# Kernel tuning notes

Hardware: AMD Instinct MI355X
Metric: run time of the kernel (lower is better)

Reference implementation:

```python
import jax, jax.numpy as jnp
import numpy as np

B, N, C, D, H, L, F = 64, 256, 16, 512, 8, 8, 2048
HD = D // H
PI = np.pi


def _ln(x, w, b, eps=1e-5):
    mu = jnp.mean(x, -1, keepdims=True)
    var = jnp.mean(jnp.square(x - mu), -1, keepdims=True)
    return (x - mu) * jax.lax.rsqrt(var + eps) * w + b


def _forward(x_node, x_full, Wp, bp, cls, e_w1, e_b1, e_w2, e_b2, edge_scale,
             qkv_w, qkv_b, out_w, out_b, ln1_w, ln1_b, ln2_w, ln2_b,
             ff1_w, ff1_b, ff2_w, ff2_b, cl_ln_w, cl_ln_b, cl_w1, cl_b1, cl_w2, cl_b2):
    Bq, Nq, _ = x_node.shape
    # pairwise kaon geometry from absolute y/phi
    y = x_full[:, :, 14]
    phi = x_full[:, :, 15]
    dy = jnp.abs(y[:, :, None] - y[:, None, :])                                  # [B,N,N]
    dphi = jnp.abs(jnp.mod(phi[:, :, None] - phi[:, None, :] + PI, 2 * PI) - PI)
    dr = jnp.sqrt(dy * dy + dphi * dphi + 1e-8)
    ef = jnp.stack([dy, dphi, dr], -1)                                           # [B,N,N,3]
    hmid = jax.nn.gelu(ef @ e_w1.T + e_b1, approximate=False)                    # [B,N,N,16]
    raw = hmid @ e_w2.T + e_b2                                                   # [B,N,N,H]
    central = jnp.mean(raw, axis=2).transpose(0, 2, 1)                           # [B,H,N]
    edge_bias = raw.transpose(0, 3, 1, 2)                                        # [B,H,N,N]
    bias = jnp.zeros((Bq, H, Nq + 1, Nq + 1), x_node.dtype)
    bias = bias.at[:, :, 1:, 1:].set(edge_bias)
    bias = bias.at[:, :, 0, 1:].set(central * edge_scale)
    bias = bias.at[:, :, 1:, 0].set(central * edge_scale)

    h = x_node @ Wp.T + bp
    h = jnp.concatenate([jnp.broadcast_to(cls, (Bq, 1, D)), h], axis=1)          # [B,S,D]
    S = Nq + 1
    scale = 1.0 / np.sqrt(HD)
    for l in range(L):  # pre-norm TransformerEncoderLayer (activation=relu, no final norm)
        x = _ln(h, ln1_w[l], ln1_b[l])
        qkv = x @ qkv_w[l].T + qkv_b[l]
        q, k, v = jnp.split(qkv, 3, axis=-1)
        q = q.reshape(Bq, S, H, HD).transpose(0, 2, 1, 3)
        k = k.reshape(Bq, S, H, HD).transpose(0, 2, 1, 3)
        v = v.reshape(Bq, S, H, HD).transpose(0, 2, 1, 3)
        scores = jnp.einsum('bhqd,bhkd->bhqk', q, k) * scale + bias
        attn = jax.nn.softmax(scores, axis=-1)
        o = jnp.einsum('bhqk,bhkd->bhqd', attn, v).transpose(0, 2, 1, 3).reshape(Bq, S, D)
        h = h + o @ out_w[l].T + out_b[l]
        x = _ln(h, ln2_w[l], ln2_b[l])
        h = h + jax.nn.relu(x @ ff1_w[l].T + ff1_b[l]) @ ff2_w[l].T + ff2_b[l]
    x = _ln(h[:, 0], cl_ln_w, cl_ln_b)
    return jax.nn.gelu(x @ cl_w1.T + cl_b1, approximate=False) @ cl_w2.T + cl_b2  # [B,2]


def setup_inputs() -> dict:
    key = jax.random.key(0)
    ks = iter(jax.random.split(key, 40))
    f32 = jnp.float32

    def nrm(shape, s=0.02):
        return (s * jax.random.normal(next(ks), shape)).astype(f32)

    return {
        'x_node': jax.random.normal(next(ks), (B, N, C), f32),
        'x_full': jax.random.normal(next(ks), (B, N, 16), f32),
        'Wp': nrm((D, C)), 'bp': jnp.zeros((D,), f32),
        'cls': nrm((1, 1, D)),
        'e_w1': nrm((16, 3), 0.3), 'e_b1': jnp.zeros((16,), f32),
        'e_w2': nrm((H, 16), 0.01), 'e_b2': jnp.zeros((H,), f32),
        'edge_scale': jnp.full((1,), 0.1, f32),
        'qkv_w': nrm((L, 3 * D, D)), 'qkv_b': jnp.zeros((L, 3 * D), f32),
        'out_w': nrm((L, D, D)), 'out_b': jnp.zeros((L, D), f32),
        'ln1_w': jnp.ones((L, D), f32), 'ln1_b': jnp.zeros((L, D), f32),
        'ln2_w': jnp.ones((L, D), f32), 'ln2_b': jnp.zeros((L, D), f32),
        'ff1_w': nrm((L, F, D)), 'ff1_b': jnp.zeros((L, F), f32),
        'ff2_w': nrm((L, D, F)), 'ff2_b': jnp.zeros((L, D), f32),
        'cl_ln_w': jnp.ones((D,), f32), 'cl_ln_b': jnp.zeros((D,), f32),
        'cl_w1': nrm((D // 2, D)), 'cl_b1': jnp.zeros((D // 2,), f32),
        'cl_w2': nrm((2, D // 2)), 'cl_b2': jnp.zeros((2,), f32),
    }


def reference(x_node, x_full, Wp, bp, cls, e_w1, e_b1, e_w2, e_b2, edge_scale,
              qkv_w, qkv_b, out_w, out_b, ln1_w, ln1_b, ln2_w, ln2_b,
              ff1_w, ff1_b, ff2_w, ff2_b, cl_ln_w, cl_ln_b, cl_w1, cl_b1, cl_w2, cl_b2):
    return _forward(x_node, x_full, Wp, bp, cls, e_w1, e_b1, e_w2, e_b2, edge_scale,
                    qkv_w, qkv_b, out_w, out_b, ln1_w, ln1_b, ln2_w, ln2_b,
                    ff1_w, ff1_b, ff2_w, ff2_b, cl_ln_w, cl_ln_b, cl_w1, cl_b1, cl_w2, cl_b2)
```

## Files before the change

kernel.cpp:

```cpp
#include <hip/hip_runtime.h>
#include <hip/hip_bf16.h>
#include <stdint.h>

#define PI_F     3.14159265358979323846f
#define TWO_PI_F 6.28318530717958647692f
#define INV2PI_F 0.15915494309189535f

typedef __attribute__((ext_vector_type(8))) short bf16x8;
typedef __attribute__((ext_vector_type(4))) float f32x4;

#define BB 64
#define NN 256
#define SS 257
#define DD 512
#define HH 8
#define HDD 64
#define LL 8
#define MTOK 16448
#define MPAD 16512
#define BSTR 264
#define VSTR 320

__device__ __forceinline__ float b2f(unsigned short u){
  union { float f; uint32_t i; } c; c.i = ((uint32_t)u) << 16; return c.f;
}
__device__ __forceinline__ unsigned short f2b(float f){
  union { float f; uint32_t i; } c; c.f = f;
  uint32_t r = c.i + 0x7FFFu + ((c.i >> 16) & 1u);
  return (unsigned short)(r >> 16);
}
__device__ __forceinline__ float gelu_fast(float z){
  const float z2 = z*z;
  const float u2 = z * (1.5957691216f + 0.071354816f*z2);
  const float e = __expf(u2);
  const float r = __builtin_amdgcn_rcpf(1.f + e);
  const float th = 1.f - 2.f*r;
  return 0.5f*z*(1.f + th);
}

typedef __attribute__((address_space(1))) unsigned char ga_t;
typedef __attribute__((address_space(3))) unsigned char ls_t;
__device__ __forceinline__ void gl_lds16(const void* g, void* l){
  __builtin_amdgcn_global_load_lds((ga_t*)g, (ls_t*)l, 16, 0, 0);
}

__global__ __launch_bounds__(256) void cvt_kernel(const float* __restrict__ src,
                                                  unsigned short* __restrict__ dst, int n2){
  int i = blockIdx.x*256 + threadIdx.x;
  int stride = gridDim.x*256;
  for (; i < n2; i += stride){
    float2 v = ((const float2*)src)[i];
    ((uint32_t*)dst)[i] = (uint32_t)f2b(v.x) | ((uint32_t)f2b(v.y) << 16);
  }
}

__global__ __launch_bounds__(256) void edge_kernel(
    const float* __restrict__ x_full, const float* __restrict__ e_w1, const float* __restrict__ e_b1,
    const float* __restrict__ e_w2, const float* __restrict__ e_b2,
    unsigned short* __restrict__ bias, float* __restrict__ central)
{
  const int bi = blockIdx.x;
  const int b = bi >> 8, i = bi & 255;
  const int j = threadIdx.x;
  const float yi = x_full[((long)b*NN + i)*16 + 14];
  const float fi = x_full[((long)b*NN + i)*16 + 15];
  const float yj = x_full[((long)b*NN + j)*16 + 14];
  const float fj = x_full[((long)b*NN + j)*16 + 15];
  const float dy = fabsf(yi - yj);
  const float xw = fi - fj + PI_F;
  const float tw = xw * INV2PI_F;
  const float md = (tw - floorf(tw)) * TWO_PI_F;
  const float dphi = fabsf(md - PI_F);
  const float dr = sqrtf(dy*dy + dphi*dphi + 1e-8f);
  float raw[8];
  #pragma unroll
  for (int hh = 0; hh < 8; ++hh) raw[hh] = e_b2[hh];
  #pragma unroll
  for (int k = 0; k < 16; ++k){
    float z = e_w1[k*3]*dy + e_w1[k*3+1]*dphi + e_w1[k*3+2]*dr + e_b1[k];
    float g = gelu_fast(z);
    #pragma unroll
    for (int hh = 0; hh < 8; ++hh) raw[hh] += g * e_w2[hh*16 + k];
  }
  #pragma unroll
  for (int hh = 0; hh < 8; ++hh)
    bias[(((long)b*HH + hh)*SS + 1 + i)*BSTR + 1 + j] = f2b(raw[hh]);
  #pragma unroll
  for (int m = 1; m < 64; m <<= 1)
    #pragma unroll
    for (int hh = 0; hh < 8; ++hh) raw[hh] += __shfl_xor(raw[hh], m);
  __shared__ float cw[4][8];
  const int wv = j >> 6;
  if ((j & 63) == 0)
    for (int hh = 0; hh < 8; ++hh) cw[wv][hh] = raw[hh];
  __syncthreads();
  if (j < 8){
    float t = cw[0][j] + cw[1][j] + cw[2][j] + cw[3][j];
    central[((long)b*NN + i)*HH + j] = t * (1.f/NN);
  }
}

__global__ __launch_bounds__(256) void edge_border_kernel(
    const float* __restrict__ central, const float* __restrict__ edge_scale,
    unsigned short* __restrict__ bias)
{
  const int bh = blockIdx.x;
  const int b = bh >> 3, h = bh & 7;
  const int j = threadIdx.x;
  const float es = edge_scale[0];
  const float cv = central[((long)b*NN + j)*HH + h] * es;
  const long base = (long)bh*SS*BSTR;
  const unsigned short u = f2b(cv);
  bias[base + 1 + j] = u;
  bias[base + (long)(1+j)*BSTR] = u;
  if (j == 0) bias[base] = 0;
}

__global__ __launch_bounds__(256) void proj_kernel(
    const float* __restrict__ x_node, const float* __restrict__ Wp,
    const float* __restrict__ bp, const float* __restrict__ cls, float* __restrict__ hb)
{
  const int t = blockIdx.x;
  const int tid = threadIdx.x;
  const int b = t / SS, s2 = t - b*SS;
  float2 o;
  if (s2 == 0){
    o = *(const float2*)(cls + tid*2);
  } else {
    const float* xr = x_node + ((long)b*NN + (s2-1))*16;
    float xv[16];
    #pragma unroll
    for (int c2 = 0; c2 < 16; ++c2) xv[c2] = xr[c2];
    float oo[2];
    #pragma unroll
    for (int e = 0; e < 2; ++e){
      int d = tid*2 + e;
      float a = bp[d];
      const float* wr2 = Wp + (long)d*16;
      #pragma unroll
      for (int c2 = 0; c2 < 16; ++c2) a += xv[c2]*wr2[c2];
      oo[e] = a;
    }
    o.x = oo[0]; o.y = oo[1];
  }
  *(float2*)(hb + (long)t*DD + tid*2) = o;
}

__global__ __launch_bounds__(256) void ln_kernel(
    const float* __restrict__ hb, const float* __restrict__ w,
    const float* __restrict__ bbv, unsigned short* __restrict__ xb)
{
  const int tok = blockIdx.x*4 + (threadIdx.x >> 6);
  const int lane = threadIdx.x & 63;
  const float4* p = (const float4*)(hb + (long)tok*DD + lane*8);
  const float4 a = p[0], bq = p[1];
  float s  = a.x + a.y + a.z + a.w + bq.x + bq.y + bq.z + bq.w;
  float ss = a.x*a.x + a.y*a.y + a.z*a.z + a.w*a.w
           + bq.x*bq.x + bq.y*bq.y + bq.z*bq.z + bq.w*bq.w;
  #pragma unroll
  for (int m = 1; m < 64; m <<= 1){ s += __shfl_xor(s, m); ss += __shfl_xor(ss, m); }
  const float mu = s * (1.f/DD);
  const float var = ss * (1.f/DD) - mu*mu;
  const float rs = rsqrtf(var + 1e-5f);
  const float4* wp = (const float4*)(w + lane*8);
  const float4* bp2 = (const float4*)(bbv + lane*8);
  const float4 w0 = wp[0], w1 = wp[1];
  const float4 b0 = bp2[0], b1 = bp2[1];
  bf16x8 o;
  o[0] = (short)f2b((a.x - mu)*rs*w0.x + b0.x);
  o[1] = (short)f2b((a.y - mu)*rs*w0.y + b0.y);
  o[2] = (short)f2b((a.z - mu)*rs*w0.z + b0.z);
  o[3] = (short)f2b((a.w - mu)*rs*w0.w + b0.w);
  o[4] = (short)f2b((bq.x - mu)*rs*w1.x + b1.x);
  o[5] = (short)f2b((bq.y - mu)*rs*w1.y + b1.y);
  o[6] = (short)f2b((bq.z - mu)*rs*w1.z + b1.z);
  o[7] = (short)f2b((bq.w - mu)*rs*w1.w + b1.w);
  *(bf16x8*)(xb + (long)tok*DD + lane*8) = o;
}

template<int EPI, int MI, int NI, int WPE>
__global__ __launch_bounds__(256, WPE) void gemm_kernel(
    const unsigned short* __restrict__ A, const unsigned short* __restrict__ Bw,
    const float* __restrict__ bias, void* __restrict__ Cout,
    int M, int N, int K, int ldc, int nblocks)
{
  __shared__ __align__(16) char smem[MI*4096 + NI*4096];
  unsigned short* As = (unsigned short*)smem;
  unsigned short* Bs = (unsigned short*)(smem + MI*4096);
  const int tid = threadIdx.x;
  const int lane = tid & 63;
  const int wave = tid >> 6;
  const int wr = wave >> 1, wc = wave & 1;
  const int l16 = lane & 15, lhi = lane >> 4;

  const int nwg = gridDim.x;
  const int q8 = nwg >> 3, r8 = nwg & 7;
  const int xcd = blockIdx.x & 7, idx = blockIdx.x >> 3;
  const int lin = (xcd < r8 ? xcd*(q8+1) : r8*(q8+1) + (xcd-r8)*q8) + idx;
  const int mb = lin / nblocks;
  const int nb = lin - mb*nblocks;
  const long m0 = (long)mb * (MI*32);
  const long n0 = (long)nb * (NI*32);

  f32x4 acc[MI][NI];
  const f32x4 z4 = {0.f, 0.f, 0.f, 0.f};
  #pragma unroll
  for (int mi = 0; mi < MI; ++mi)
    #pragma unroll
    for (int ni = 0; ni < NI; ++ni) acc[mi][ni] = z4;

  const char* Ab = (const char*)A;
  const char* Bb = (const char*)Bw;
  const int nkt = K >> 6;
  for (int kt = 0; kt < nkt; ++kt){
    #pragma unroll
    for (int c = 0; c < MI; ++c){
      const int bo = c*4096 + tid*16;
      const int row = bo >> 7;
      const int kb = bo & 127;
      gl_lds16(Ab + ((m0+row)*(long)K)*2 + (long)kt*128 + kb, (char*)As + bo);
    }
    #pragma unroll
    for (int c = 0; c < NI; ++c){
      const int bo = c*4096 + tid*16;
      const int row = bo >> 7;
      const int kb = bo & 127;
      gl_lds16(Bb + ((n0+row)*(long)K)*2 + (long)kt*128 + kb, (char*)Bs + bo);
    }
    __syncthreads();
    #pragma unroll
    for (int kd = 0; kd < 2; ++kd){
      bf16x8 af[MI], bfr[NI];
      #pragma unroll
      for (int mi = 0; mi < MI; ++mi)
        af[mi] = *(const bf16x8*)((const char*)As + (wr*(MI*16) + mi*16 + l16)*128 + kd*64 + lhi*16);
      #pragma unroll
      for (int ni = 0; ni < NI; ++ni)
        bfr[ni] = *(const bf16x8*)((const char*)Bs + (wc*(NI*16) + ni*16 + l16)*128 + kd*64 + lhi*16);
      #pragma unroll
      for (int mi = 0; mi < MI; ++mi)
        #pragma unroll
        for (int ni = 0; ni < NI; ++ni)
          acc[mi][ni] = __builtin_amdgcn_mfma_f32_16x16x32_bf16(af[mi], bfr[ni], acc[mi][ni], 0, 0, 0);
    }
    __syncthreads();
  }

  if (EPI == 2){
    float* Cs = (float*)smem;
    const int NC = NI*32;
    const int LDSC = NC + 4;
    float* Cg = (float*)Cout;
    #pragma unroll
    for (int half = 0; half < 2; ++half){
      if (wr == half){
        #pragma unroll
        for (int mi = 0; mi < MI; ++mi)
          #pragma unroll
          for (int ni = 0; ni < NI; ++ni){
            const int col = wc*(NI*16) + ni*16 + l16;
            #pragma unroll
            for (int r = 0; r < 4; ++r)
              Cs[(mi*16 + lhi*4 + r)*LDSC + col] = acc[mi][ni][r];
          }
      }
      __syncthreads();
      #pragma unroll
      for (int it = 0; it < MI; ++it){
        const int idx = tid + it*256;
        const int c4 = idx & 15;
        const int row = idx >> 4;
        const int gm = (int)m0 + half*(MI*16) + row;
        if (gm < M){
          const long go = (long)gm*ldc + n0 + c4*4;
          float4 cv = *(float4*)&Cg[go];
          const float* ls = &Cs[row*LDSC + c4*4];
          const float4 bv = *(const float4*)&bias[n0 + c4*4];
          cv.x += ls[0] + bv.x; cv.y += ls[1] + bv.y;
          cv.z += ls[2] + bv.z; cv.w += ls[3] + bv.w;
          *(float4*)&Cg[go] = cv;
        }
      }
      __syncthreads();
    }
  } else {
    #pragma unroll
    for (int mi = 0; mi < MI; ++mi){
      #pragma unroll
      for (int ni = 0; ni < NI; ++ni){
        const int col = (int)n0 + wc*(NI*16) + ni*16 + l16;
        const float bn = bias[col];
        const int rowb = (int)m0 + wr*(MI*16) + mi*16 + lhi*4;
        #pragma unroll
        for (int r = 0; r < 4; ++r){
          const int m = rowb + r;
          if (m < M){
            float v = acc[mi][ni][r] + bn;
            if (EPI == 1) v = fmaxf(v, 0.f);
            ((unsigned short*)Cout)[(long)m*ldc + col] = f2b(v);
          }
        }
      }
    }
  }
}

__global__ __launch_bounds__(256) void vtrans_kernel(
    const unsigned short* __restrict__ qkv, unsigned short* __restrict__ vt)
{
  const int bh = blockIdx.x;
  const int c = blockIdx.y;
  const int b = bh >> 3, h = bh & 7;
  __shared__ unsigned short tile[64][72];
  const int tid = threadIdx.x;
  const int rr = tid >> 3, ch = tid & 7;
  #pragma unroll
  for (int it = 0; it < 2; ++it){
    const int sl = it*32 + rr;
    const long tok = (long)b*SS + c*64 + sl;
    bf16x8 v = *(const bf16x8*)(qkv + tok*1536 + 1024 + h*64 + ch*8);
    *(bf16x8*)(&tile[sl][ch*8]) = v;
  }
  __syncthreads();
  #pragma unroll
  for (int it = 0; it < 2; ++it){
    const int d = it*32 + rr;
    const int s0 = c*64 + ch*8;
    bf16x8 o;
    #pragma unroll
    for (int e = 0; e < 8; ++e){
      const int sgl = s0 + e;
      o[e] = (sgl < SS) ? (short)tile[ch*8 + e][d] : (short)0;
    }
    *(bf16x8*)(vt + ((long)bh*HDD + d)*VSTR + s0) = o;
  }
}

__global__ __launch_bounds__(576) void flash_kernel(
    const unsigned short* __restrict__ qkv, const unsigned short* __restrict__ vt,
    const unsigned short* __restrict__ bias, unsigned short* __restrict__ ob)
{
  const int bh = blockIdx.x;
  const int b = bh >> 3, h = bh & 7;
  const int qt = threadIdx.x >> 6;
  const int lane = threadIdx.x & 63;
  const int l16 = lane & 15, lhi = lane >> 4;

  __shared__ unsigned short Ks[2][2048];
  __shared__ unsigned short Vs[2][2048];
  __shared__ unsigned short Bsh[9][2][1024];
  __shared__ unsigned short pt[9][1024];
  unsigned short* ptw = pt[qt];

  bf16x8 qf[2][2];
  #pragma unroll
  for (int mi = 0; mi < 2; ++mi)
    #pragma unroll
    for (int kd = 0; kd < 2; ++kd){
      const long tok = (long)b*SS + qt*32 + mi*16 + l16;
      qf[mi][kd] = *(const bf16x8*)(qkv + tok*1536 + h*64 + kd*32 + lhi*8);
    }

  auto stage = [&](int jtn, int bb){
    const int rB = lane >> 2, cB = lane & 3;
    const char* gb = (const char*)bias + (((long)bh*SS + qt*32)*BSTR + (long)jtn*32)*2;
    char* lb = (char*)&Bsh[qt][bb][0];
    gl_lds16(gb + (long)rB*BSTR*2        + cB*16, lb + lane*16);
    gl_lds16(gb + (long)(16+rB)*BSTR*2   + cB*16, lb + 1024 + lane*16);
    if (qt < 4){
      const int rK = lane >> 3, cK = lane & 7;
      gl_lds16((const char*)qkv + (((long)b*SS + jtn*32 + qt*8 + rK)*1536 + 512 + h*64)*2 + ((cK ^ rK)*16),
               (char*)&Ks[bb][0] + qt*1024 + lane*16);
    } else if (qt < 8){
      const int rV = lane >> 2, cV = lane & 3;
      const int d = (qt-4)*16 + rV;
      gl_lds16((const char*)vt + (((long)bh*64 + d)*VSTR + (long)jtn*32)*2 + ((cV ^ (rV & 3))*16),
               (char*)&Vs[bb][0] + (qt-4)*1024 + lane*16);
    }
  };

  f32x4 oacc[2][4];
  const f32x4 z4 = {0.f, 0.f, 0.f, 0.f};
  #pragma unroll
  for (int mi = 0; mi < 2; ++mi)
    #pragma unroll
    for (int ni = 0; ni < 4; ++ni) oacc[mi][ni] = z4;
  float mrow[2][4], lrow[2][4];
  #pragma unroll
  for (int mi = 0; mi < 2; ++mi)
    #pragma unroll
    for (int r = 0; r < 4; ++r){ mrow[mi][r] = -1e30f; lrow[mi][r] = 0.f; }

  stage(0, 0);
  __builtin_amdgcn_sched_barrier(0);

  for (int jt = 0; jt < 9; ++jt){
    const int cur = jt & 1;
    if (jt < 8){
      stage(jt+1, cur ^ 1);
      __builtin_amdgcn_sched_barrier(0);
      if (qt < 8) asm volatile("s_waitcnt vmcnt(3)" ::: "memory");
      else        asm volatile("s_waitcnt vmcnt(2)" ::: "memory");
    } else {
      asm volatile("s_waitcnt vmcnt(0)" ::: "memory");
    }
    __builtin_amdgcn_sched_barrier(0);
    __builtin_amdgcn_s_barrier();
    __builtin_amdgcn_sched_barrier(0);

    bf16x8 kf[2][2];
    #pragma unroll
    for (int ni = 0; ni < 2; ++ni)
      #pragma unroll
      for (int kd = 0; kd < 2; ++kd){
        const int row = ni*16 + l16;
        const int sw = (kd*4 + lhi) ^ (row & 7);
        kf[ni][kd] = *(const bf16x8*)((const char*)&Ks[cur][0] + row*128 + sw*16);
      }
    f32x4 sacc[2][2];
    #pragma unroll
    for (int mi = 0; mi < 2; ++mi)
      #pragma unroll
      for (int ni = 0; ni < 2; ++ni) sacc[mi][ni] = z4;
    __builtin_amdgcn_s_setprio(1);
    #pragma unroll
    for (int kd = 0; kd < 2; ++kd)
      #pragma unroll
      for (int mi = 0; mi < 2; ++mi)
        #pragma unroll
        for (int ni = 0; ni < 2; ++ni)
          sacc[mi][ni] = __builtin_amdgcn_mfma_f32_16x16x32_bf16(qf[mi][kd], kf[ni][kd], sacc[mi][ni], 0, 0, 0);
    __builtin_amdgcn_s_setprio(0);

    float sv[2][2][4];
    #pragma unroll
    for (int mi = 0; mi < 2; ++mi)
      #pragma unroll
      for (int ni = 0; ni < 2; ++ni)
        #pragma unroll
        for (int r = 0; r < 4; ++r){
          const int col = jt*32 + ni*16 + l16;
          float x = sacc[mi][ni][r] * 0.125f;
          x += b2f(Bsh[qt][cur][(mi*16 + lhi*4 + r)*32 + ni*16 + l16]);
          if (col >= SS) x = -1e30f;
          sv[mi][ni][r] = x;
        }
    #pragma unroll
    for (int mi = 0; mi < 2; ++mi)
      #pragma unroll
      for (int r = 0; r < 4; ++r){
        float pm = fmaxf(sv[mi][0][r], sv[mi][1][r]);
        #pragma unroll
        for (int sh = 1; sh < 16; sh <<= 1) pm = fmaxf(pm, __shfl_xor(pm, sh));
        const float mold = mrow[mi][r];
        const float mnew = fmaxf(mold, pm);
        const float corr = __expf(mold - mnew);
        mrow[mi][r] = mnew;
        float psum = 0.f;
        #pragma unroll
        for (int ni = 0; ni < 2; ++ni){
          const float p = __expf(sv[mi][ni][r] - mnew);
          sv[mi][ni][r] = p;
          psum += p;
        }
        #pragma unroll
        for (int sh = 1; sh < 16; sh <<= 1) psum += __shfl_xor(psum, sh);
        lrow[mi][r] = lrow[mi][r]*corr + psum;
        #pragma unroll
        for (int ni = 0; ni < 4; ++ni) oacc[mi][ni][r] = oacc[mi][ni][r]*corr;
      }
    #pragma unroll
    for (int mi = 0; mi < 2; ++mi)
      #pragma unroll
      for (int ni = 0; ni < 2; ++ni)
        #pragma unroll
        for (int r = 0; r < 4; ++r)
          ptw[(mi*16 + lhi*4 + r)*32 + ni*16 + l16] = f2b(sv[mi][ni][r]);
    bf16x8 pf[2];
    #pragma unroll
    for (int mi = 0; mi < 2; ++mi)
      pf[mi] = *(const bf16x8*)(ptw + (mi*16 + l16)*32 + lhi*8);
    bf16x8 vf[4];
    #pragma unroll
    for (int ni = 0; ni < 4; ++ni){
      const int d = ni*16 + l16;
      const int sw = lhi ^ (d & 3);
      vf[ni] = *(const bf16x8*)((const char*)&Vs[cur][0] + d*64 + sw*16);
    }
    __builtin_amdgcn_s_setprio(1);
    #pragma unroll
    for (int mi = 0; mi < 2; ++mi)
      #pragma unroll
      for (int ni = 0; ni < 4; ++ni)
        oacc[mi][ni] = __builtin_amdgcn_mfma_f32_16x16x32_bf16(pf[mi], vf[ni], oacc[mi][ni], 0, 0, 0);
    __builtin_amdgcn_s_setprio(0);

    __builtin_amdgcn_sched_barrier(0);
    __builtin_amdgcn_s_barrier();
    __builtin_amdgcn_sched_barrier(0);
  }

  #pragma unroll
  for (int mi = 0; mi < 2; ++mi)
    #pragma unroll
    for (int r = 0; r < 4; ++r){
      const int row = qt*32 + mi*16 + lhi*4 + r;
      if (row < SS){
        const float inv = 1.0f / lrow[mi][r];
        const long tok = (long)b*SS + row;
        #pragma unroll
        for (int ni = 0; ni < 4; ++ni)
          ob[tok*DD + h*HDD + ni*16 + l16] = f2b(oacc[mi][ni][r] * inv);
      }
    }
}

__global__ __launch_bounds__(256) void cls_kernel(
    const float* __restrict__ hb, const float* __restrict__ lw, const float* __restrict__ lb,
    const float* __restrict__ w1, const float* __restrict__ b1,
    const float* __restrict__ w2, const float* __restrict__ b2, float* __restrict__ out)
{
  const int b = blockIdx.x;
  const int tid = threadIdx.x;
  const float* row = hb + (long)b*SS*DD;
  const float2 v = *(const float2*)(row + tid*2);
  float s = v.x + v.y, ss = v.x*v.x + v.y*v.y;
  #pragma unroll
  for (int m = 1; m < 64; m <<= 1){ s += __shfl_xor(s, m); ss += __shfl_xor(ss, m); }
  __shared__ float red[8];
  const int wv = tid >> 6;
  if ((tid & 63) == 0){ red[wv] = s; red[4+wv] = ss; }
  __syncthreads();
  s  = red[0]+red[1]+red[2]+red[3];
  ss = red[4]+red[5]+red[6]+red[7];
  const float mu = s * (1.f/DD);
  const float var = ss * (1.f/DD) - mu*mu;
  const float rs = rsqrtf(var + 1e-5f);
  __shared__ __align__(16) float xs[DD];
  xs[tid*2]   = (v.x - mu)*rs*lw[tid*2]   + lb[tid*2];
  xs[tid*2+1] = (v.y - mu)*rs*lw[tid*2+1] + lb[tid*2+1];
  __syncthreads();
  float a = b1[tid];
  const float4* w1v = (const float4*)(w1 + (long)tid*DD);
  const float4* xsv = (const float4*)xs;
  for (int d4 = 0; d4 < DD/4; ++d4){
    const float4 wv4 = w1v[d4], xv4 = xsv[d4];
    a += wv4.x*xv4.x + wv4.y*xv4.y + wv4.z*xv4.z + wv4.w*xv4.w;
  }
  const float g = 0.5f*a*(1.f + erff(a*0.70710678118f));
  float p0 = g * w2[tid];
  float p1 = g * w2[256 + tid];
  #pragma unroll
  for (int m = 1; m < 64; m <<= 1){ p0 += __shfl_xor(p0, m); p1 += __shfl_xor(p1, m); }
  __shared__ float r2[8];
  if ((tid & 63) == 0){ r2[wv] = p0; r2[4+wv] = p1; }
  __syncthreads();
  if (tid == 0) out[b*2]   = r2[0]+r2[1]+r2[2]+r2[3] + b2[0];
  if (tid == 1) out[b*2+1] = r2[4]+r2[5]+r2[6]+r2[7] + b2[1];
}

extern "C" void kernel_launch(void* const* d_in, const int* in_sizes, int n_in,
                              void* d_out, int out_size, void* d_ws, size_t ws_size,
                              hipStream_t stream) {
  const float* x_node    = (const float*)d_in[0];
  const float* x_full    = (const float*)d_in[1];
  const float* Wp        = (const float*)d_in[2];
  const float* bp        = (const float*)d_in[3];
  const float* cls       = (const float*)d_in[4];
  const float* e_w1      = (const float*)d_in[5];
  const float* e_b1      = (const float*)d_in[6];
  const float* e_w2      = (const float*)d_in[7];
  const float* e_b2      = (const float*)d_in[8];
  const float* edge_scale= (const float*)d_in[9];
  const float* qkv_w     = (const float*)d_in[10];
  const float* qkv_b     = (const float*)d_in[11];
  const float* out_w     = (const float*)d_in[12];
  const float* out_b     = (const float*)d_in[13];
  const float* ln1_w     = (const float*)d_in[14];
  const float* ln1_b     = (const float*)d_in[15];
  const float* ln2_w     = (const float*)d_in[16];
  const float* ln2_b     = (const float*)d_in[17];
  const float* ff1_w     = (const float*)d_in[18];
  const float* ff1_b     = (const float*)d_in[19];
  const float* ff2_w     = (const float*)d_in[20];
  const float* ff2_b     = (const float*)d_in[21];
  const float* cl_ln_w   = (const float*)d_in[22];
  const float* cl_ln_b   = (const float*)d_in[23];
  const float* cl_w1     = (const float*)d_in[24];
  const float* cl_b1     = (const float*)d_in[25];
  const float* cl_w2     = (const float*)d_in[26];
  const float* cl_b2     = (const float*)d_in[27];
  float* out = (float*)d_out;

  char* w = (char*)d_ws;
  size_t off = 0;
  auto take = [&](size_t bytes)->char*{
    char* p = w + off;
    off += (bytes + 255) & ~(size_t)255;
    return p;
  };
  unsigned short* wq8   = (unsigned short*)take((size_t)LL*1536*512*2);
  unsigned short* wo8   = (unsigned short*)take((size_t)LL*512*512*2);
  unsigned short* wf1   = (unsigned short*)take((size_t)LL*2048*512*2);
  unsigned short* wf2   = (unsigned short*)take((size_t)LL*512*2048*2);
  unsigned short* bias16= (unsigned short*)take((size_t)BB*HH*SS*BSTR*2 + 65536);
  float*          cent  = (float*)take((size_t)BB*NN*HH*4);
  float*          hbuf  = (float*)take((size_t)MPAD*DD*4);
  unsigned short* xb    = (unsigned short*)take((size_t)MPAD*DD*2);
  unsigned short* obuf  = (unsigned short*)take((size_t)MPAD*DD*2);
  unsigned short* qkvb  = (unsigned short*)take((size_t)MPAD*1536*2);
  unsigned short* vtb   = (unsigned short*)take((size_t)BB*HH*HDD*VSTR*2);
  unsigned short* ffb   = qkvb;

  cvt_kernel<<<4096, 256, 0, stream>>>(qkv_w, wq8, LL*1536*512/2);
  cvt_kernel<<<4096, 256, 0, stream>>>(out_w, wo8, LL*512*512/2);
  cvt_kernel<<<4096, 256, 0, stream>>>(ff1_w, wf1, LL*2048*512/2);
  cvt_kernel<<<4096, 256, 0, stream>>>(ff2_w, wf2, LL*512*2048/2);

  edge_kernel<<<dim3(BB*NN), 256, 0, stream>>>(x_full, e_w1, e_b1, e_w2, e_b2, bias16, cent);
  edge_border_kernel<<<dim3(BB*HH), 256, 0, stream>>>(cent, edge_scale, bias16);
  proj_kernel<<<dim3(MTOK), 256, 0, stream>>>(x_node, Wp, bp, cls, hbuf);

  for (int l = 0; l < LL; ++l){
    ln_kernel<<<dim3(MTOK/4), 256, 0, stream>>>(hbuf, ln1_w + l*DD, ln1_b + l*DD, xb);
    gemm_kernel<0,4,4,4><<<dim3(129*12), 256, 0, stream>>>(xb, wq8 + (size_t)l*1536*512,
        qkv_b + (size_t)l*1536, qkvb, MTOK, 1536, 512, 1536, 12);
    vtrans_kernel<<<dim3(512, 5), 256, 0, stream>>>(qkvb, vtb);
    flash_kernel<<<dim3(512), 576, 0, stream>>>(qkvb, vtb, bias16, obuf);
    gemm_kernel<2,4,2,6><<<dim3(129*8), 256, 0, stream>>>(obuf, wo8 + (size_t)l*512*512,
        out_b + (size_t)l*DD, hbuf, MTOK, 512, 512, 512, 8);
    ln_kernel<<<dim3(MTOK/4), 256, 0, stream>>>(hbuf, ln2_w + l*DD, ln2_b + l*DD, xb);
    gemm_kernel<1,4,4,4><<<dim3(129*16), 256, 0, stream>>>(xb, wf1 + (size_t)l*2048*512,
        ff1_b + (size_t)l*2048, ffb, MTOK, 2048, 512, 2048, 16);
    gemm_kernel<2,4,2,6><<<dim3(129*8), 256, 0, stream>>>(ffb, wf2 + (size_t)l*512*2048,
        ff2_b + (size_t)l*DD, hbuf, MTOK, 512, 2048, 512, 8);
  }
  cls_kernel<<<dim3(BB), 256, 0, stream>>>(hbuf, cl_ln_w, cl_ln_b, cl_w1, cl_b1, cl_w2, cl_b2, out);
}
```

Measured before the change: 2.530 ms.

## Prepack attention bias into MFMA fragment layout and load it into registers

A new one-time kernel repacks the padded bf16 attention bias into per-tile, per-lane MFMA accumulator order. The flash kernel then reads each lane's bias values with two coalesced 16-byte register loads, prefetched one KV tile ahead, instead of staging bias through shared memory and reading it back element by element. This removes the large bias LDS buffer, so more of the CU's shared memory is free and the LDS traffic per tile drops. In exchange there are more live registers, a larger bias workspace, and the original bias and output buffers now alias the qkv and LN-output workspaces.

```diff
diff --git a/kernel.cpp b/kernel.cpp
--- a/kernel.cpp
+++ b/kernel.cpp
@@ -114,6 +114,28 @@
   bias[base + 1 + j] = u;
   bias[base + (long)(1+j)*BSTR] = u;
   if (j == 0) bias[base] = 0;
+}
+
+__global__ __launch_bounds__(256) void brepack_kernel(
+    const unsigned short* __restrict__ biasO, unsigned short* __restrict__ biasT)
+{
+  const int bh = blockIdx.x;
+  const int qt = blockIdx.y;
+  const int t = threadIdx.x;
+  const int ln = t & 63, wv = t >> 6;
+  const int l16 = ln & 15, lhi = ln >> 4;
+  for (int c = wv; c < 18; c += 4){
+    const int jt = c >> 1, mi = c & 1;
+    bf16x8 v;
+    #pragma unroll
+    for (int idx8 = 0; idx8 < 8; ++idx8){
+      const int ni = idx8 >> 2, r = idx8 & 3;
+      int row = qt*32 + mi*16 + lhi*4 + r; if (row > 256) row = 256;
+      int col = jt*32 + ni*16 + l16;       if (col > 263) col = 263;
+      v[idx8] = (short)biasO[((long)bh*SS + row)*BSTR + col];
+    }
+    *(bf16x8*)(biasT + ((((long)bh*9 + qt)*9 + jt)*2 + mi)*512 + ln*8) = v;
+  }
 }
 
 __global__ __launch_bounds__(256) void proj_kernel(
@@ -338,7 +360,7 @@
 
 __global__ __launch_bounds__(576) void flash_kernel(
     const unsigned short* __restrict__ qkv, const unsigned short* __restrict__ vt,
-    const unsigned short* __restrict__ bias, unsigned short* __restrict__ ob)
+    const unsigned short* __restrict__ biasT, unsigned short* __restrict__ ob)
 {
   const int bh = blockIdx.x;
   const int b = bh >> 3, h = bh & 7;
@@ -348,7 +370,6 @@
 
   __shared__ unsigned short Ks[2][2048];
   __shared__ unsigned short Vs[2][2048];
-  __shared__ unsigned short Bsh[9][2][1024];
   __shared__ unsigned short pt[9][1024];
   unsigned short* ptw = pt[qt];
 
@@ -362,11 +383,6 @@
     }
 
   auto stage = [&](int jtn, int bb){
-    const int rB = lane >> 2, cB = lane & 3;
-    const char* gb = (const char*)bias + (((long)bh*SS + qt*32)*BSTR + (long)jtn*32)*2;
-    char* lb = (char*)&Bsh[qt][bb][0];
-    gl_lds16(gb + (long)rB*BSTR*2        + cB*16, lb + lane*16);
-    gl_lds16(gb + (long)(16+rB)*BSTR*2   + cB*16, lb + 1024 + lane*16);
     if (qt < 4){
       const int rK = lane >> 3, cK = lane & 7;
       gl_lds16((const char*)qkv + (((long)b*SS + jtn*32 + qt*8 + rK)*1536 + 512 + h*64)*2 + ((cK ^ rK)*16),
@@ -379,6 +395,12 @@
     }
   };
 
+  const long tqb = ((long)bh*9 + qt)*9;
+  bf16x8 btA0, btA1, btB0, btB1;
+  btA0 = *(const bf16x8*)(biasT + (tqb + 0)*1024 + lane*8);
+  btA1 = *(const bf16x8*)(biasT + (tqb + 0)*1024 + 512 + lane*8);
+  btB0 = btA0; btB1 = btA1;
+
   f32x4 oacc[2][4];
   const f32x4 z4 = {0.f, 0.f, 0.f, 0.f};
   #pragma unroll
@@ -398,6 +420,14 @@
     const int cur = jt & 1;
     if (jt < 8){
       stage(jt+1, cur ^ 1);
+      const long tbn = (tqb + (jt+1))*1024;
+      if (cur){
+        btA0 = *(const bf16x8*)(biasT + tbn + lane*8);
+        btA1 = *(const bf16x8*)(biasT + tbn + 512 + lane*8);
+      } else {
+        btB0 = *(const bf16x8*)(biasT + tbn + lane*8);
+        btB1 = *(const bf16x8*)(biasT + tbn + 512 + lane*8);
+      }
       __builtin_amdgcn_sched_barrier(0);
       if (qt < 8) asm volatile("s_waitcnt vmcnt(3)" ::: "memory");
       else        asm volatile("s_waitcnt vmcnt(2)" ::: "memory");
@@ -407,6 +437,9 @@
     __builtin_amdgcn_sched_barrier(0);
     __builtin_amdgcn_s_barrier();
     __builtin_amdgcn_sched_barrier(0);
+
+    const bf16x8 bt0 = cur ? btB0 : btA0;
+    const bf16x8 bt1 = cur ? btB1 : btA1;
 
     bf16x8 kf[2][2];
     #pragma unroll
@@ -441,7 +474,7 @@
         for (int r = 0; r < 4; ++r){
           const int col = jt*32 + ni*16 + l16;
           float x = sacc[mi][ni][r] * 0.125f;
-          x += b2f(Bsh[qt][cur][(mi*16 + lhi*4 + r)*32 + ni*16 + l16]);
+          x += b2f((unsigned short)((mi ? bt1 : bt0)[ni*4 + r]));
           if (col >= SS) x = -1e30f;
           sv[mi][ni][r] = x;
         }
@@ -603,14 +636,15 @@
   unsigned short* wo8   = (unsigned short*)take((size_t)LL*512*512*2);
   unsigned short* wf1   = (unsigned short*)take((size_t)LL*2048*512*2);
   unsigned short* wf2   = (unsigned short*)take((size_t)LL*512*2048*2);
-  unsigned short* bias16= (unsigned short*)take((size_t)BB*HH*SS*BSTR*2 + 65536);
+  unsigned short* biasT = (unsigned short*)take((size_t)512*81*1024*2);
   float*          cent  = (float*)take((size_t)BB*NN*HH*4);
   float*          hbuf  = (float*)take((size_t)MPAD*DD*4);
   unsigned short* xb    = (unsigned short*)take((size_t)MPAD*DD*2);
-  unsigned short* obuf  = (unsigned short*)take((size_t)MPAD*DD*2);
   unsigned short* qkvb  = (unsigned short*)take((size_t)MPAD*1536*2);
   unsigned short* vtb   = (unsigned short*)take((size_t)BB*HH*HDD*VSTR*2);
   unsigned short* ffb   = qkvb;
+  unsigned short* bias16= qkvb;
+  unsigned short* obuf  = xb;
 
   cvt_kernel<<<4096, 256, 0, stream>>>(qkv_w, wq8, LL*1536*512/2);
   cvt_kernel<<<4096, 256, 0, stream>>>(out_w, wo8, LL*512*512/2);
@@ -619,6 +653,7 @@
 
   edge_kernel<<<dim3(BB*NN), 256, 0, stream>>>(x_full, e_w1, e_b1, e_w2, e_b2, bias16, cent);
   edge_border_kernel<<<dim3(BB*HH), 256, 0, stream>>>(cent, edge_scale, bias16);
+  brepack_kernel<<<dim3(512, 9), 256, 0, stream>>>(bias16, biasT);
   proj_kernel<<<dim3(MTOK), 256, 0, stream>>>(x_node, Wp, bp, cls, hbuf);
 
   for (int l = 0; l < LL; ++l){
@@ -626,7 +661,7 @@
     gemm_kernel<0,4,4,4><<<dim3(129*12), 256, 0, stream>>>(xb, wq8 + (size_t)l*1536*512,
         qkv_b + (size_t)l*1536, qkvb, MTOK, 1536, 512, 1536, 12);
     vtrans_kernel<<<dim3(512, 5), 256, 0, stream>>>(qkvb, vtb);
-    flash_kernel<<<dim3(512), 576, 0, stream>>>(qkvb, vtb, bias16, obuf);
+    flash_kernel<<<dim3(512), 576, 0, stream>>>(qkvb, vtb, biasT, obuf);
     gemm_kernel<2,4,2,6><<<dim3(129*8), 256, 0, stream>>>(obuf, wo8 + (size_t)l*512*512,
         out_b + (size_t)l*DD, hbuf, MTOK, 512, 512, 512, 8);
     ln_kernel<<<dim3(MTOK/4), 256, 0, stream>>>(hbuf, ln2_w + l*DD, ln2_b + l*DD, xb);
```

New measurement: 2.559 ms. Within noise of the previous version (+1.1%).
